# Kernel tuning notes

Hardware: AMD Instinct MI355X
Metric: run time of the kernel (lower is better)

The kernel has to match this reference:

```python
import jax, jax.numpy as jnp
import numpy as np

B, T, D = 1, 4096, 768
H, HD = 12, 64  # num_heads, head_dim; H*HD == D


def setup_inputs() -> dict:
    key = jax.random.key(0)
    ks = jax.random.split(key, 12)
    s = 1.0 / np.sqrt(D)  # nn.Linear-style init scale
    inp = {
        "query": jax.random.normal(ks[0], (B, T, D), jnp.float32),
        "key": jax.random.normal(ks[1], (B, T, D), jnp.float32),
        "value": jax.random.normal(ks[2], (B, T, D), jnp.float32),
        # causal mask: True positions are masked (strict upper triangle)
        "mask": jnp.triu(jnp.ones((T, T), dtype=bool), k=1),
        "Wq_w": jax.random.normal(ks[3], (D, D), jnp.float32) * s,
        "Wq_b": jax.random.normal(ks[4], (D,), jnp.float32) * s,
        "Wk_w": jax.random.normal(ks[5], (D, D), jnp.float32) * s,
        "Wk_b": jax.random.normal(ks[6], (D,), jnp.float32) * s,
        "Wv_w": jax.random.normal(ks[7], (D, D), jnp.float32) * s,
        "Wv_b": jax.random.normal(ks[8], (D,), jnp.float32) * s,
        "W0_w": jax.random.normal(ks[9], (D, D), jnp.float32) * s,
        "W0_b": jax.random.normal(ks[10], (D,), jnp.float32) * s,
    }
    return inp


def _split_heads(x):
    # (B, T, D) -> (B, H, T, HD)
    b, t, _ = x.shape
    return x.reshape(b, t, H, HD).transpose(0, 2, 1, 3)


def reference(query, key, value, mask, Wq_w, Wq_b, Wk_w, Wk_b, Wv_w, Wv_b, W0_w, W0_b):
    # Q/K/V projections (torch Linear: x @ W.T + b)
    q = _split_heads(query @ Wq_w.T + Wq_b)
    k = _split_heads(key @ Wk_w.T + Wk_b)
    v = _split_heads(value @ Wv_w.T + Wv_b)

    scale = 1.0 / jnp.sqrt(jnp.asarray(HD, q.dtype))
    scores = jnp.einsum("bhqd,bhkd->bhqk", q, k) * scale  # (B,H,T,T)
    scores = jnp.where(mask, -jnp.inf, scores)
    weights = jax.nn.softmax(scores, axis=-1)  # (B,H,T,T)
    attn = jnp.einsum("bhqk,bhkd->bhqd", weights, v)  # (B,H,T,HD)

    # concat heads: (B,H,T,HD) -> (B,T,D), then output projection
    out = attn.transpose(0, 2, 1, 3).reshape(query.shape[0], -1, D)
    output = out @ W0_w.T + W0_b
    return output, weights
```

## Files before the change

kernel.cpp:

```cpp
#include <hip/hip_runtime.h>

#define TSEQ 4096
#define DM 768
#define NHEAD 12
#define HDIM 64
#define SC 0.1803368801111204f

using f32x4  = __attribute__((ext_vector_type(4))) float;
using bf16x8 = __attribute__((ext_vector_type(8))) short;
using bf16x4 = __attribute__((ext_vector_type(4))) short;

#define LGKM_BARRIER() asm volatile("s_waitcnt lgkmcnt(0)\n\ts_barrier" ::: "memory")

__device__ __forceinline__ short f2bf(float f) {
    union { float f; unsigned u; } x; x.f = f;
    unsigned r = x.u + 0x7FFFu + ((x.u >> 16) & 1u);
    return (short)(r >> 16);
}

__device__ __forceinline__ unsigned pk2(float lo, float hi) {
    unsigned d;
    asm("v_cvt_pk_bf16_f32 %0, %1, %2" : "=v"(d) : "v"(lo), "v"(hi));
    return d;
}

__device__ __forceinline__ bf16x8 pack8(f32x4 a, f32x4 b) {
    union { unsigned u[4]; bf16x8 v; } r;
    r.u[0] = pk2(a[0], a[1]); r.u[1] = pk2(a[2], a[3]);
    r.u[2] = pk2(b[0], b[1]); r.u[3] = pk2(b[2], b[3]);
    return r.v;
}

__device__ __forceinline__ f32x4 mfma16(bf16x8 a, bf16x8 b, f32x4 c) {
    return __builtin_amdgcn_mfma_f32_16x16x32_bf16(a, b, c, 0, 0, 0);
}

__global__ __launch_bounds__(512) void gemm_qkv(
    const float* __restrict__ q_in, const float* __restrict__ k_in,
    const float* __restrict__ v_in,
    const float* __restrict__ Wq_w, const float* __restrict__ Wq_b,
    const float* __restrict__ Wk_w, const float* __restrict__ Wk_b,
    const float* __restrict__ Wv_w, const float* __restrict__ Wv_b,
    short* __restrict__ Qb, short* __restrict__ Kb, short* __restrict__ Vt)
{
    constexpr int K = DM;
    __shared__ __align__(16) short As[64 * 72];
    __shared__ __align__(16) short Bs[256 * 72];

    const int D = blockIdx.x;
    const int o = (D & 7) * 72 + (D >> 3);
    const int bm = (o & 63) * 64;
    const int g  = o >> 6;
    const int bn = (g % 3) * 256;
    const int z  = g / 3;

    const float* A    = (z == 0) ? q_in : (z == 1) ? k_in : v_in;
    const float* W    = (z == 0) ? Wq_w : (z == 1) ? Wk_w : Wv_w;
    const float* bias = (z == 0) ? Wq_b : (z == 1) ? Wk_b : Wv_b;

    const int tid = threadIdx.x;
    const int wid = tid >> 6;
    const int lane = tid & 63;
    const int wm = wid >> 2, wn = wid & 3;
    const int l15 = lane & 15, lq = lane >> 4;

    f32x4 acc[2][4] = {};
    const int sr = tid >> 3;
    const int sc = (tid & 7) * 8;

    for (int k0 = 0; k0 < K; k0 += 64) {
        {
            const float* ga = A + (size_t)(bm + sr) * K + k0 + sc;
            *(bf16x8*)&As[sr * 72 + sc] =
                pack8(*(const f32x4*)ga, *(const f32x4*)(ga + 4));
        }
        #pragma unroll
        for (int it = 0; it < 4; ++it) {
            int r = sr + it * 64;
            const float* gb = W + (size_t)(bn + r) * K + k0 + sc;
            *(bf16x8*)&Bs[r * 72 + sc] =
                pack8(*(const f32x4*)gb, *(const f32x4*)(gb + 4));
        }
        LGKM_BARRIER();
        __builtin_amdgcn_s_setprio(1);
        #pragma unroll
        for (int ks = 0; ks < 2; ++ks) {
            bf16x8 af0 = *(bf16x8*)&As[(wm * 32 + l15) * 72 + ks * 32 + lq * 8];
            bf16x8 af1 = *(bf16x8*)&As[(wm * 32 + 16 + l15) * 72 + ks * 32 + lq * 8];
            #pragma unroll
            for (int n = 0; n < 4; ++n) {
                bf16x8 bfv = *(bf16x8*)&Bs[(wn * 64 + n * 16 + l15) * 72 + ks * 32 + lq * 8];
                acc[0][n] = mfma16(af0, bfv, acc[0][n]);
                acc[1][n] = mfma16(af1, bfv, acc[1][n]);
            }
        }
        __builtin_amdgcn_s_setprio(0);
        LGKM_BARRIER();
    }

    #pragma unroll
    for (int mf = 0; mf < 2; ++mf) {
        const int row0 = bm + wm * 32 + mf * 16 + lq * 4;
        #pragma unroll
        for (int n = 0; n < 4; ++n) {
            int col = bn + wn * 64 + n * 16 + l15;
            float b = bias[col];
            if (z == 2) {
                uint2 pv;
                pv.x = pk2(acc[mf][n][0] + b, acc[mf][n][1] + b);
                pv.y = pk2(acc[mf][n][2] + b, acc[mf][n][3] + b);
                *(uint2*)(Vt + (size_t)col * TSEQ + row0) = pv;
            } else {
                short* dst = (z == 0) ? Qb : Kb;
                #pragma unroll
                for (int r = 0; r < 4; ++r)
                    dst[(size_t)(row0 + r) * DM + col] = f2bf(acc[mf][n][r] + b);
            }
        }
    }
}

__global__ __launch_bounds__(512) void gemm_out(
    const float* __restrict__ A, const float* __restrict__ W,
    const float* __restrict__ bias, float* __restrict__ Cout)
{
    constexpr int K = DM;
    __shared__ __align__(16) short As[64 * 72];
    __shared__ __align__(16) short Bs[256 * 72];

    const int D = blockIdx.x;
    const int o = (D & 7) * 24 + (D >> 3);
    const int bm = (o & 63) * 64;
    const int bn = (o >> 6) * 256;

    const int tid = threadIdx.x;
    const int wid = tid >> 6;
    const int lane = tid & 63;
    const int wm = wid >> 2, wn = wid & 3;
    const int l15 = lane & 15, lq = lane >> 4;

    f32x4 acc[2][4] = {};
    const int sr = tid >> 3;
    const int sc = (tid & 7) * 8;

    for (int k0 = 0; k0 < K; k0 += 64) {
        {
            const float* ga = A + (size_t)(bm + sr) * K + k0 + sc;
            *(bf16x8*)&As[sr * 72 + sc] =
                pack8(*(const f32x4*)ga, *(const f32x4*)(ga + 4));
        }
        #pragma unroll
        for (int it = 0; it < 4; ++it) {
            int r = sr + it * 64;
            const float* gb = W + (size_t)(bn + r) * K + k0 + sc;
            *(bf16x8*)&Bs[r * 72 + sc] =
                pack8(*(const f32x4*)gb, *(const f32x4*)(gb + 4));
        }
        LGKM_BARRIER();
        __builtin_amdgcn_s_setprio(1);
        #pragma unroll
        for (int ks = 0; ks < 2; ++ks) {
            bf16x8 af0 = *(bf16x8*)&As[(wm * 32 + l15) * 72 + ks * 32 + lq * 8];
            bf16x8 af1 = *(bf16x8*)&As[(wm * 32 + 16 + l15) * 72 + ks * 32 + lq * 8];
            #pragma unroll
            for (int n = 0; n < 4; ++n) {
                bf16x8 bfv = *(bf16x8*)&Bs[(wn * 64 + n * 16 + l15) * 72 + ks * 32 + lq * 8];
                acc[0][n] = mfma16(af0, bfv, acc[0][n]);
                acc[1][n] = mfma16(af1, bfv, acc[1][n]);
            }
        }
        __builtin_amdgcn_s_setprio(0);
        LGKM_BARRIER();
    }

    #pragma unroll
    for (int mf = 0; mf < 2; ++mf) {
        const int row0 = bm + wm * 32 + mf * 16 + lq * 4;
        #pragma unroll
        for (int n = 0; n < 4; ++n) {
            int col = bn + wn * 64 + n * 16 + l15;
            float b = bias[col];
            #pragma unroll
            for (int r = 0; r < 4; ++r)
                Cout[(size_t)(row0 + r) * DM + col] = acc[mf][n][r] + b;
        }
    }
}

__global__ __launch_bounds__(256) void attn_fused(
    const short* __restrict__ Qb, const short* __restrict__ Kb,
    const short* __restrict__ Vt, float* __restrict__ Wout,
    float* __restrict__ AttnO)
{
    const int bid = blockIdx.x;
    const int j = bid & 63;
    const int s = bid >> 8;
    const int h = s * 4 + ((bid >> 6) & 3);
    const int qt = (s == 0) ? j
                 : (s == 1) ? ((j + 32) & 63)
                 : ((j < 32) ? 62 - 2 * j : 127 - 2 * j);
    const int q0 = qt * 64;
    const int tid = threadIdx.x, wid = tid >> 6, lane = tid & 63;
    const int l15 = lane & 15, lq = lane >> 4;

    __shared__ __align__(16) short lds[23040];

    const int nkt = qt + 1;

    {
        float* wbase = Wout + (size_t)h * TSEQ * TSEQ + (size_t)(q0 + wid * 16) * TSEQ;
        f32x4 z = {0.f, 0.f, 0.f, 0.f};
        for (int kt = nkt; kt < 64; ++kt) {
            #pragma unroll
            for (int i = 0; i < 4; ++i)
                __builtin_nontemporal_store(
                    z, (f32x4*)(wbase + (size_t)(lq + i * 4) * TSEQ + kt * 64 + l15 * 4));
        }
    }

    const short* qp = Qb + (size_t)(q0 + wid * 16 + l15) * DM + h * HDIM + lq * 8;
    bf16x8 qf0 = *(const bf16x8*)qp;
    bf16x8 qf1 = *(const bf16x8*)(qp + 32);

    const short* kbase = Kb + (size_t)h * HDIM;
    const short* vbase = Vt + (size_t)h * HDIM * TSEQ;
    const int myq = q0 + wid * 16 + l15;

    const int srow = tid >> 3;
    const int scol = (tid & 7) * 8;

    const int nch = (nkt + 1) >> 1;
    auto stageKbig = [&](int c, int b) {
        const int base_k = c * 128;
        const int iters = (nkt * 64 - base_k) >= 128 ? 4 : 2;
        short* dst = lds + b * (128 * 72);
        for (int it = 0; it < iters; ++it) {
            int r = srow + it * 32;
            *(bf16x8*)&dst[r * 72 + scol] =
                *(const bf16x8*)&kbase[(size_t)(base_k + r) * DM + scol];
        }
    };

    f32x4 lacc = {0.f, 0.f, 0.f, 0.f};
    stageKbig(0, 0);
    LGKM_BARRIER();
    for (int c = 0; c < nch; ++c) {
        const int b = c & 1;
        if (c + 1 < nch) stageKbig(c + 1, b ^ 1);
        const short* kb = lds + b * (128 * 72);
        #pragma unroll
        for (int t = 0; t < 2; ++t) {
            const int kt = c * 2 + t;
            if (kt >= nkt) break;
            f32x4 s4[4] = {};
            __builtin_amdgcn_s_setprio(1);
            #pragma unroll
            for (int ks = 0; ks < 2; ++ks) {
                bf16x8 qf = ks ? qf1 : qf0;
                #pragma unroll
                for (int n = 0; n < 4; ++n) {
                    bf16x8 kf = *(const bf16x8*)
                        &kb[(t * 64 + n * 16 + l15) * 72 + ks * 32 + lq * 8];
                    s4[n] = mfma16(kf, qf, s4[n]);
                }
            }
            __builtin_amdgcn_s_setprio(0);
            if (kt == qt) {
                #pragma unroll
                for (int n = 0; n < 4; ++n) {
                    int kb0 = kt * 64 + n * 16 + lq * 4;
                    #pragma unroll
                    for (int r = 0; r < 4; ++r)
                        lacc[n] += (kb0 + r <= myq) ? exp2f(s4[n][r] * SC) : 0.f;
                }
            } else {
                #pragma unroll
                for (int n = 0; n < 4; ++n)
                    #pragma unroll
                    for (int r = 0; r < 4; ++r)
                        lacc[n] += exp2f(s4[n][r] * SC);
            }
        }
        LGKM_BARRIER();
    }
    float lsum = (lacc[0] + lacc[1]) + (lacc[2] + lacc[3]);
    lsum += __shfl_xor(lsum, 16);
    lsum += __shfl_xor(lsum, 32);
    const float nlog = -__log2f(lsum);

    short* Ks2 = lds;
    short* Vs2 = lds + 2 * 64 * 72;
    short* Psw = lds + 4 * 64 * 72 + wid * (16 * 72);

    bf16x8 krg0, krg1, vrg0, vrg1;
    auto loadKV = [&](int kt) {
        krg0 = *(const bf16x8*)&kbase[(size_t)(kt * 64 + srow) * DM + scol];
        krg1 = *(const bf16x8*)&kbase[(size_t)(kt * 64 + srow + 32) * DM + scol];
        vrg0 = *(const bf16x8*)&vbase[(size_t)srow * TSEQ + kt * 64 + scol];
        vrg1 = *(const bf16x8*)&vbase[(size_t)(srow + 32) * TSEQ + kt * 64 + scol];
    };
    auto writeKV = [&](int b) {
        short* kd = Ks2 + b * (64 * 72);
        short* vd = Vs2 + b * (64 * 72);
        *(bf16x8*)&kd[srow * 72 + scol] = krg0;
        *(bf16x8*)&kd[(srow + 32) * 72 + scol] = krg1;
        *(bf16x8*)&vd[srow * 72 + scol] = vrg0;
        *(bf16x8*)&vd[(srow + 32) * 72 + scol] = vrg1;
    };

    float* wq = Wout + (size_t)h * TSEQ * TSEQ + (size_t)myq * TSEQ;
    f32x4 o[4] = {};
    loadKV(0);
    writeKV(0);
    LGKM_BARRIER();
    for (int kt = 0; kt < nkt; ++kt) {
        const int b = kt & 1;
        const bool more = (kt + 1 < nkt);
        if (more) {
            loadKV(kt + 1);
            __builtin_amdgcn_sched_barrier(0);
        }
        f32x4 s4[4] = {};
        __builtin_amdgcn_s_setprio(1);
        #pragma unroll
        for (int ks = 0; ks < 2; ++ks) {
            bf16x8 qf = ks ? qf1 : qf0;
            #pragma unroll
            for (int n = 0; n < 4; ++n) {
                bf16x8 kf = *(const bf16x8*)
                    &Ks2[b * (64 * 72) + (n * 16 + l15) * 72 + ks * 32 + lq * 8];
                s4[n] = mfma16(kf, qf, s4[n]);
            }
        }
        __builtin_amdgcn_s_setprio(0);
        const bool diag = (kt == qt);
        #pragma unroll
        for (int n = 0; n < 4; ++n) {
            const int kb0 = kt * 64 + n * 16 + lq * 4;
            f32x4 p;
            #pragma unroll
            for (int r = 0; r < 4; ++r) {
                float e = exp2f(fmaf(s4[n][r], SC, nlog));
                p[r] = (diag && (kb0 + r > myq)) ? 0.f : e;
            }
            *(f32x4*)(wq + kb0) = p;
            uint2 pv;
            pv.x = pk2(p[0], p[1]);
            pv.y = pk2(p[2], p[3]);
            *(uint2*)&Psw[l15 * 72 + n * 16 + lq * 4] = pv;
        }
        __builtin_amdgcn_s_setprio(1);
        #pragma unroll
        for (int ks = 0; ks < 2; ++ks) {
            bf16x8 pf = *(bf16x8*)&Psw[l15 * 72 + ks * 32 + lq * 8];
            #pragma unroll
            for (int n = 0; n < 4; ++n) {
                bf16x8 vf = *(const bf16x8*)
                    &Vs2[b * (64 * 72) + (n * 16 + l15) * 72 + ks * 32 + lq * 8];
                o[n] = mfma16(pf, vf, o[n]);
            }
        }
        __builtin_amdgcn_s_setprio(0);
        if (more) {
            __builtin_amdgcn_sched_barrier(0);
            writeKV(b ^ 1);
        }
        LGKM_BARRIER();
    }

    #pragma unroll
    for (int n = 0; n < 4; ++n) {
        int col = h * HDIM + n * 16 + l15;
        #pragma unroll
        for (int r = 0; r < 4; ++r) {
            int row = q0 + wid * 16 + lq * 4 + r;
            AttnO[(size_t)row * DM + col] = o[n][r];
        }
    }
}

extern "C" void kernel_launch(void* const* d_in, const int* in_sizes, int n_in,
                              void* d_out, int out_size, void* d_ws, size_t ws_size,
                              hipStream_t stream)
{
    const float* q_in = (const float*)d_in[0];
    const float* k_in = (const float*)d_in[1];
    const float* v_in = (const float*)d_in[2];
    const float* Wq_w = (const float*)d_in[4];
    const float* Wq_b = (const float*)d_in[5];
    const float* Wk_w = (const float*)d_in[6];
    const float* Wk_b = (const float*)d_in[7];
    const float* Wv_w = (const float*)d_in[8];
    const float* Wv_b = (const float*)d_in[9];
    const float* W0_w = (const float*)d_in[10];
    const float* W0_b = (const float*)d_in[11];

    float* out  = (float*)d_out;
    float* wout = out + (size_t)TSEQ * DM;

    short* Qb = (short*)d_ws;
    short* Kb = Qb + (size_t)TSEQ * DM;
    short* Vt = Kb + (size_t)TSEQ * DM;
    float* AttnO = (float*)(Vt + (size_t)TSEQ * DM);

    gemm_qkv<<<576, 512, 0, stream>>>(
        q_in, k_in, v_in, Wq_w, Wq_b, Wk_w, Wk_b, Wv_w, Wv_b, Qb, Kb, Vt);
    attn_fused<<<768, 256, 0, stream>>>(Qb, Kb, Vt, wout, AttnO);
    gemm_out<<<192, 512, 0, stream>>>(AttnO, W0_w, W0_b, out);
}
```

Measured before the change: 310.8 us.

## Load V fragments directly from global memory instead of LDS staging

```diff
diff --git a/kernel.cpp b/kernel.cpp
--- a/kernel.cpp
+++ b/kernel.cpp
@@ -187,7 +187,7 @@
     }
 }
 
-__global__ __launch_bounds__(256) void attn_fused(
+__global__ __launch_bounds__(256, 4) void attn_fused(
     const short* __restrict__ Qb, const short* __restrict__ Kb,
     const short* __restrict__ Vt, float* __restrict__ Wout,
     float* __restrict__ AttnO)
@@ -203,7 +203,7 @@
     const int tid = threadIdx.x, wid = tid >> 6, lane = tid & 63;
     const int l15 = lane & 15, lq = lane >> 4;
 
-    __shared__ __align__(16) short lds[23040];
+    __shared__ __align__(16) short lds[18432];
 
     const int nkt = qt + 1;
 
@@ -289,35 +289,29 @@
     const float nlog = -__log2f(lsum);
 
     short* Ks2 = lds;
-    short* Vs2 = lds + 2 * 64 * 72;
-    short* Psw = lds + 4 * 64 * 72 + wid * (16 * 72);
-
-    bf16x8 krg0, krg1, vrg0, vrg1;
-    auto loadKV = [&](int kt) {
+    short* Psw = lds + 2 * 64 * 72 + wid * (16 * 72);
+
+    bf16x8 krg0, krg1;
+    auto loadK = [&](int kt) {
         krg0 = *(const bf16x8*)&kbase[(size_t)(kt * 64 + srow) * DM + scol];
         krg1 = *(const bf16x8*)&kbase[(size_t)(kt * 64 + srow + 32) * DM + scol];
-        vrg0 = *(const bf16x8*)&vbase[(size_t)srow * TSEQ + kt * 64 + scol];
-        vrg1 = *(const bf16x8*)&vbase[(size_t)(srow + 32) * TSEQ + kt * 64 + scol];
     };
-    auto writeKV = [&](int b) {
+    auto writeK = [&](int b) {
         short* kd = Ks2 + b * (64 * 72);
-        short* vd = Vs2 + b * (64 * 72);
         *(bf16x8*)&kd[srow * 72 + scol] = krg0;
         *(bf16x8*)&kd[(srow + 32) * 72 + scol] = krg1;
-        *(bf16x8*)&vd[srow * 72 + scol] = vrg0;
-        *(bf16x8*)&vd[(srow + 32) * 72 + scol] = vrg1;
     };
 
     float* wq = Wout + (size_t)h * TSEQ * TSEQ + (size_t)myq * TSEQ;
     f32x4 o[4] = {};
-    loadKV(0);
-    writeKV(0);
+    loadK(0);
+    writeK(0);
     LGKM_BARRIER();
     for (int kt = 0; kt < nkt; ++kt) {
         const int b = kt & 1;
         const bool more = (kt + 1 < nkt);
         if (more) {
-            loadKV(kt + 1);
+            loadK(kt + 1);
             __builtin_amdgcn_sched_barrier(0);
         }
         f32x4 s4[4] = {};
@@ -333,6 +327,16 @@
             }
         }
         __builtin_amdgcn_s_setprio(0);
+        const short* vkt = vbase + kt * 64 + lq * 8;
+        bf16x8 vfa0 = *(const bf16x8*)&vkt[(size_t)(l15)      * TSEQ];
+        bf16x8 vfa1 = *(const bf16x8*)&vkt[(size_t)(16 + l15) * TSEQ];
+        bf16x8 vfa2 = *(const bf16x8*)&vkt[(size_t)(32 + l15) * TSEQ];
+        bf16x8 vfa3 = *(const bf16x8*)&vkt[(size_t)(48 + l15) * TSEQ];
+        bf16x8 vfb0 = *(const bf16x8*)&vkt[(size_t)(l15)      * TSEQ + 32];
+        bf16x8 vfb1 = *(const bf16x8*)&vkt[(size_t)(16 + l15) * TSEQ + 32];
+        bf16x8 vfb2 = *(const bf16x8*)&vkt[(size_t)(32 + l15) * TSEQ + 32];
+        bf16x8 vfb3 = *(const bf16x8*)&vkt[(size_t)(48 + l15) * TSEQ + 32];
+
         const bool diag = (kt == qt);
         #pragma unroll
         for (int n = 0; n < 4; ++n) {
@@ -350,20 +354,22 @@
             *(uint2*)&Psw[l15 * 72 + n * 16 + lq * 4] = pv;
         }
         __builtin_amdgcn_s_setprio(1);
-        #pragma unroll
-        for (int ks = 0; ks < 2; ++ks) {
-            bf16x8 pf = *(bf16x8*)&Psw[l15 * 72 + ks * 32 + lq * 8];
-            #pragma unroll
-            for (int n = 0; n < 4; ++n) {
-                bf16x8 vf = *(const bf16x8*)
-                    &Vs2[b * (64 * 72) + (n * 16 + l15) * 72 + ks * 32 + lq * 8];
-                o[n] = mfma16(pf, vf, o[n]);
-            }
+        {
+            bf16x8 pf0 = *(bf16x8*)&Psw[l15 * 72 + lq * 8];
+            bf16x8 pf1 = *(bf16x8*)&Psw[l15 * 72 + 32 + lq * 8];
+            o[0] = mfma16(pf0, vfa0, o[0]);
+            o[1] = mfma16(pf0, vfa1, o[1]);
+            o[2] = mfma16(pf0, vfa2, o[2]);
+            o[3] = mfma16(pf0, vfa3, o[3]);
+            o[0] = mfma16(pf1, vfb0, o[0]);
+            o[1] = mfma16(pf1, vfb1, o[1]);
+            o[2] = mfma16(pf1, vfb2, o[2]);
+            o[3] = mfma16(pf1, vfb3, o[3]);
         }
         __builtin_amdgcn_s_setprio(0);
         if (more) {
             __builtin_amdgcn_sched_barrier(0);
-            writeKV(b ^ 1);
+            writeK(b ^ 1);
         }
         LGKM_BARRIER();
     }
```

New measurement: 352.1 us (median of 5 runs). 1.13x slower.

## Single-buffer V in LDS, spread zero-fill stores across pass one, raise occupancy

Applied to the files above, without the earlier changes.

```diff
diff --git a/kernel.cpp b/kernel.cpp
--- a/kernel.cpp
+++ b/kernel.cpp
@@ -187,7 +187,7 @@
     }
 }
 
-__global__ __launch_bounds__(256) void attn_fused(
+__global__ __launch_bounds__(256, 4) void attn_fused(
     const short* __restrict__ Qb, const short* __restrict__ Kb,
     const short* __restrict__ Vt, float* __restrict__ Wout,
     float* __restrict__ AttnO)
@@ -203,20 +203,9 @@
     const int tid = threadIdx.x, wid = tid >> 6, lane = tid & 63;
     const int l15 = lane & 15, lq = lane >> 4;
 
-    __shared__ __align__(16) short lds[23040];
+    __shared__ __align__(16) short lds[18432];
 
     const int nkt = qt + 1;
-
-    {
-        float* wbase = Wout + (size_t)h * TSEQ * TSEQ + (size_t)(q0 + wid * 16) * TSEQ;
-        f32x4 z = {0.f, 0.f, 0.f, 0.f};
-        for (int kt = nkt; kt < 64; ++kt) {
-            #pragma unroll
-            for (int i = 0; i < 4; ++i)
-                __builtin_nontemporal_store(
-                    z, (f32x4*)(wbase + (size_t)(lq + i * 4) * TSEQ + kt * 64 + l15 * 4));
-        }
-    }
 
     const short* qp = Qb + (size_t)(q0 + wid * 16 + l15) * DM + h * HDIM + lq * 8;
     bf16x8 qf0 = *(const bf16x8*)qp;
@@ -240,6 +229,11 @@
                 *(const bf16x8*)&kbase[(size_t)(base_k + r) * DM + scol];
         }
     };
+
+    float* wzero = Wout + (size_t)h * TSEQ * TSEQ + (size_t)(q0 + wid * 16) * TSEQ;
+    const int zcnt = 64 - nkt;
+    int zdone = 0;
+    const f32x4 zv = {0.f, 0.f, 0.f, 0.f};
 
     f32x4 lacc = {0.f, 0.f, 0.f, 0.f};
     stageKbig(0, 0);
@@ -281,6 +275,17 @@
                         lacc[n] += exp2f(s4[n][r] * SC);
             }
         }
+        {
+            const int zgoal = (int)(((long)(c + 1) * zcnt) / nch);
+            for (; zdone < zgoal; ++zdone) {
+                const int kt = nkt + zdone;
+                #pragma unroll
+                for (int i = 0; i < 4; ++i)
+                    __builtin_nontemporal_store(
+                        zv, (f32x4*)(wzero + (size_t)(lq + i * 4) * TSEQ
+                                     + kt * 64 + l15 * 4));
+            }
+        }
         LGKM_BARRIER();
     }
     float lsum = (lacc[0] + lacc[1]) + (lacc[2] + lacc[3]);
@@ -289,8 +294,8 @@
     const float nlog = -__log2f(lsum);
 
     short* Ks2 = lds;
-    short* Vs2 = lds + 2 * 64 * 72;
-    short* Psw = lds + 4 * 64 * 72 + wid * (16 * 72);
+    short* Vs  = lds + 2 * 64 * 72;
+    short* Psw = lds + 3 * 64 * 72 + wid * (16 * 72);
 
     bf16x8 krg0, krg1, vrg0, vrg1;
     auto loadKV = [&](int kt) {
@@ -299,19 +304,21 @@
         vrg0 = *(const bf16x8*)&vbase[(size_t)srow * TSEQ + kt * 64 + scol];
         vrg1 = *(const bf16x8*)&vbase[(size_t)(srow + 32) * TSEQ + kt * 64 + scol];
     };
-    auto writeKV = [&](int b) {
+    auto writeK = [&](int b) {
         short* kd = Ks2 + b * (64 * 72);
-        short* vd = Vs2 + b * (64 * 72);
         *(bf16x8*)&kd[srow * 72 + scol] = krg0;
         *(bf16x8*)&kd[(srow + 32) * 72 + scol] = krg1;
-        *(bf16x8*)&vd[srow * 72 + scol] = vrg0;
-        *(bf16x8*)&vd[(srow + 32) * 72 + scol] = vrg1;
+    };
+    auto writeV = [&]() {
+        *(bf16x8*)&Vs[srow * 72 + scol] = vrg0;
+        *(bf16x8*)&Vs[(srow + 32) * 72 + scol] = vrg1;
     };
 
     float* wq = Wout + (size_t)h * TSEQ * TSEQ + (size_t)myq * TSEQ;
     f32x4 o[4] = {};
     loadKV(0);
-    writeKV(0);
+    writeK(0);
+    writeV();
     LGKM_BARRIER();
     for (int kt = 0; kt < nkt; ++kt) {
         const int b = kt & 1;
@@ -356,14 +363,16 @@
             #pragma unroll
             for (int n = 0; n < 4; ++n) {
                 bf16x8 vf = *(const bf16x8*)
-                    &Vs2[b * (64 * 72) + (n * 16 + l15) * 72 + ks * 32 + lq * 8];
+                    &Vs[(n * 16 + l15) * 72 + ks * 32 + lq * 8];
                 o[n] = mfma16(pf, vf, o[n]);
             }
         }
         __builtin_amdgcn_s_setprio(0);
         if (more) {
             __builtin_amdgcn_sched_barrier(0);
-            writeKV(b ^ 1);
+            LGKM_BARRIER();
+            writeK(b ^ 1);
+            writeV();
         }
         LGKM_BARRIER();
     }
```

Measured after the change: 299.9 us. -3.5%, faster.
